# Performance work log

Measured on AMD Instinct MI355X. Metric: run time of the kernel, lower is better.

Reference implementation:

```python
import jax, jax.numpy as jnp
import numpy as np

P = 16  # num_partitions
DIN = 256  # in_features // P
DOUT = 256  # out_features // P

def setup_inputs() -> dict:
    key = jax.random.key(0)
    k1, k2, k3 = jax.random.split(key, 3)
    inputs = jax.random.normal(k1, (8, 2048, P * DIN), dtype=jnp.float32)
    weight = jax.random.normal(k2, (P, DOUT, DIN), dtype=jnp.float32) * (1.0 / np.sqrt(DIN))
    bias = jax.random.normal(k3, (P * DOUT,), dtype=jnp.float32) * (1.0 / np.sqrt(DIN))
    return {"inputs": inputs, "weight": weight, "bias": bias}

def reference(inputs, weight, bias):
    # inputs: (B, S, P*DIN) -> (B, S, P, DIN)
    x = inputs.reshape(*inputs.shape[:-1], P, DIN)
    # block-diagonal matmul: (B,S,P,DIN) x (P,DOUT,DIN) -> (B,S,P,DOUT)
    y = jnp.einsum('bspi,poi->bspo', x, weight)
    # transpose=True: swap (P, DOUT) -> (DOUT, P), then flatten
    y = jnp.swapaxes(y, -2, -1)
    y = y.reshape(*y.shape[:-2], DOUT * P)
    return y + bias
```

## Files before the change

kernel.cpp:

```cpp
#include <hip/hip_runtime.h>


typedef __attribute__((ext_vector_type(4))) float f32x4;
typedef __attribute__((ext_vector_type(8))) short short8;

#define LDS_ROW 8208
#define LDS_SIZE (16 * LDS_ROW)

__device__ __forceinline__ unsigned int pk2(float a, float b) {
  union { float f; unsigned int u; } x, y;
  x.f = a; y.f = b;
  unsigned int ua = x.u + (0x7fffu + ((x.u >> 16) & 1u));
  unsigned int ub = y.u + (0x7fffu + ((y.u >> 16) & 1u));
  return (ua >> 16) | (ub & 0xffff0000u);
}

__global__ __launch_bounds__(256) void wconv_kernel(
    const float* __restrict__ w, unsigned int* __restrict__ o) {
  int i = blockIdx.x * 256 + threadIdx.x;
  float4 f = ((const float4*)w)[i];
  uint2 u;
  u.x = pk2(f.x, f.y);
  u.y = pk2(f.z, f.w);
  ((uint2*)o)[i] = u;
}

__global__ __launch_bounds__(512, 2) void diag_gemm_kernel(
    const float* __restrict__ x, const unsigned short* __restrict__ wb,
    const float* __restrict__ bias, float* __restrict__ out) {
  extern __shared__ char lds[];
  const int tid = threadIdx.x;
  const int wv  = tid >> 6;
  const int l   = tid & 63;
  const long T0 = (long)blockIdx.x * 16;

  const int n  = l & 15;
  const int kg = l >> 4;

  const unsigned short* bbs0 = wb + (wv * 16 + n) * 256 + kg * 8;
  const unsigned short* bbs1 = wb + ((wv + 8) * 16 + n) * 256 + kg * 8;

  short8 a[2][8], b[2][8];

#pragma unroll
  for (int ks = 0; ks < 8; ++ks) b[0][ks] = *(const short8*)(bbs0 + ks * 32);

#pragma unroll
  for (int rr = 0; rr < 2; ++rr) {
    const int row = wv * 2 + rr;
    const float* src = x + (T0 + row) * 4096;
    char* dst = lds + row * LDS_ROW;
#pragma unroll
    for (int i = 0; i < 8; ++i) {
      int c = l + 64 * i;
      float4 f0 = ((const float4*)src)[2 * c];
      float4 f1 = ((const float4*)src)[2 * c + 1];
      uint4 u;
      u.x = pk2(f0.x, f0.y);
      u.y = pk2(f0.z, f0.w);
      u.z = pk2(f1.x, f1.y);
      u.w = pk2(f1.z, f1.w);
      *(uint4*)(dst + c * 16) = u;
    }
  }
  __syncthreads();

  const char* abase = lds + n * LDS_ROW + kg * 16;
#pragma unroll
  for (int ks = 0; ks < 8; ++ks) a[0][ks] = *(const short8*)(abase + ks * 64);

  float* obase = out + T0 * 4096;

#pragma unroll
  for (int s = 0; s < 2; ++s) {
    const int o0 = (wv + 8 * s) * 16;
    f32x4 res[16];

#pragma unroll
    for (int p = 0; p < 16; ++p) {
      const int g = s * 16 + p;
      const int cur = g & 1, nxt = cur ^ 1;
      if (g < 31) {
        const int gn = g + 1;
        const unsigned short* bp =
            ((gn & 16) ? bbs1 : bbs0) + (gn & 15) * 65536;
#pragma unroll
        for (int ks = 0; ks < 8; ++ks)
          b[nxt][ks] = *(const short8*)(bp + ks * 32);
        const char* ap = abase + (gn & 15) * 512;
#pragma unroll
        for (int ks = 0; ks < 8; ++ks)
          a[nxt][ks] = *(const short8*)(ap + ks * 64);
      }
      f32x4 acc = (f32x4){0.f, 0.f, 0.f, 0.f};
#pragma unroll
      for (int ks = 0; ks < 8; ++ks)
        acc = __builtin_amdgcn_mfma_f32_16x16x32_bf16(a[cur][ks], b[cur][ks],
                                                      acc, 0, 0, 0);
      res[p] = acc;
    }

    const float* bp2 = bias + (o0 + n) * 16;
    float4 bv0 = ((const float4*)bp2)[0];
    float4 bv1 = ((const float4*)bp2)[1];
    float4 bv2 = ((const float4*)bp2)[2];
    float4 bv3 = ((const float4*)bp2)[3];
    float* ob = obase + (long)(o0 + n) * 16;
#pragma unroll
    for (int r = 0; r < 4; ++r) {
      float* orow = ob + (long)(kg * 4 + r) * 4096;
      float4 v0 = make_float4(res[0][r] + bv0.x, res[1][r] + bv0.y,
                              res[2][r] + bv0.z, res[3][r] + bv0.w);
      float4 v1 = make_float4(res[4][r] + bv1.x, res[5][r] + bv1.y,
                              res[6][r] + bv1.z, res[7][r] + bv1.w);
      float4 v2 = make_float4(res[8][r] + bv2.x, res[9][r] + bv2.y,
                              res[10][r] + bv2.z, res[11][r] + bv2.w);
      float4 v3 = make_float4(res[12][r] + bv3.x, res[13][r] + bv3.y,
                              res[14][r] + bv3.z, res[15][r] + bv3.w);
      ((float4*)orow)[0] = v0;
      ((float4*)orow)[1] = v1;
      ((float4*)orow)[2] = v2;
      ((float4*)orow)[3] = v3;
    }
  }
}

extern "C" void kernel_launch(void* const* d_in, const int* in_sizes, int n_in,
                              void* d_out, int out_size, void* d_ws, size_t ws_size,
                              hipStream_t stream) {
  const float* x    = (const float*)d_in[0];
  const float* w    = (const float*)d_in[1];
  const float* bias = (const float*)d_in[2];
  float* out = (float*)d_out;
  unsigned int* wb = (unsigned int*)d_ws;

  (void)hipFuncSetAttribute((const void*)diag_gemm_kernel,
                            hipFuncAttributeMaxDynamicSharedMemorySize, LDS_SIZE);

  wconv_kernel<<<1024, 256, 0, stream>>>(w, wb);

  diag_gemm_kernel<<<1024, 512, LDS_SIZE, stream>>>(
      x, (const unsigned short*)wb, bias, out);
}
```

Baseline: 672.8 us.

## Stream fp32 activation slices into LDS via async DMA with a four-buffer ring

Instead of loading all 16 token rows to registers, converting them to bf16 and storing to LDS up front, the kernel now uses global_load_lds to DMA fp32 partition slices straight into a 4-deep LDS ring buffer. Each slice is prefetched three iterations ahead and synchronised with explicit vmcnt waits and barriers. Conversion to bf16 moves to the LDS-read side using the hardware v_cvt_pk_bf16_f32 instruction. Blocks shrink to 256 threads, with each wave covering 4 output groups. The aim is to overlap global activation loads with MFMA work and cut LDS footprint, at the cost of more barriers per block and more conversions per fragment read.

```diff
diff --git a/kernel.cpp b/kernel.cpp
--- a/kernel.cpp
+++ b/kernel.cpp
@@ -4,8 +4,10 @@
 typedef __attribute__((ext_vector_type(4))) float f32x4;
 typedef __attribute__((ext_vector_type(8))) short short8;
 
-#define LDS_ROW 8208
-#define LDS_SIZE (16 * LDS_ROW)
+#define SLICE_STRIDE 1040
+#define BUF_BYTES    (16 * SLICE_STRIDE)
+#define NBUF         4
+#define LDS_TOTAL    (NBUF * BUF_BYTES)
 
 __device__ __forceinline__ unsigned int pk2(float a, float b) {
   union { float f; unsigned int u; } x, y;
@@ -13,6 +15,18 @@
   unsigned int ua = x.u + (0x7fffu + ((x.u >> 16) & 1u));
   unsigned int ub = y.u + (0x7fffu + ((y.u >> 16) & 1u));
   return (ua >> 16) | (ub & 0xffff0000u);
+}
+
+__device__ __forceinline__ unsigned int cvtpk(float a, float b) {
+  unsigned int r;
+  asm("v_cvt_pk_bf16_f32 %0, %1, %2" : "=v"(r) : "v"(a), "v"(b));
+  return r;
+}
+
+__device__ __forceinline__ void dma_row(const float* g, char* l) {
+  __builtin_amdgcn_global_load_lds(
+      (const __attribute__((address_space(1))) unsigned int*)g,
+      (__attribute__((address_space(3))) unsigned int*)l, 16, 0, 0);
 }
 
 __global__ __launch_bounds__(256) void wconv_kernel(
@@ -25,7 +39,7 @@
   ((uint2*)o)[i] = u;
 }
 
-__global__ __launch_bounds__(512, 2) void diag_gemm_kernel(
+__global__ __launch_bounds__(256, 2) void diag_gemm_kernel(
     const float* __restrict__ x, const unsigned short* __restrict__ wb,
     const float* __restrict__ bias, float* __restrict__ out) {
   extern __shared__ char lds[];
@@ -37,69 +51,85 @@
   const int n  = l & 15;
   const int kg = l >> 4;
 
-  const unsigned short* bbs0 = wb + (wv * 16 + n) * 256 + kg * 8;
-  const unsigned short* bbs1 = wb + ((wv + 8) * 16 + n) * 256 + kg * 8;
+  const int C0 = (wv * 16 + n) * 256 + kg * 8;
+  const float* xrow0 = x + (T0 + wv * 4) * 4096 + l * 4;
 
-  short8 a[2][8], b[2][8];
+  short8 a[8], b[2][8];
 
 #pragma unroll
-  for (int ks = 0; ks < 8; ++ks) b[0][ks] = *(const short8*)(bbs0 + ks * 32);
-
+  for (int sl = 0; sl < 3; ++sl) {
 #pragma unroll
-  for (int rr = 0; rr < 2; ++rr) {
-    const int row = wv * 2 + rr;
-    const float* src = x + (T0 + row) * 4096;
-    char* dst = lds + row * LDS_ROW;
+    for (int i = 0; i < 4; ++i)
+      dma_row(xrow0 + i * 4096 + sl * 256,
+              lds + sl * BUF_BYTES + (wv * 4 + i) * SLICE_STRIDE);
+  }
+  __builtin_amdgcn_sched_barrier(0);
+  {
+    const unsigned short* bp = wb + C0;
 #pragma unroll
-    for (int i = 0; i < 8; ++i) {
-      int c = l + 64 * i;
-      float4 f0 = ((const float4*)src)[2 * c];
-      float4 f1 = ((const float4*)src)[2 * c + 1];
-      uint4 u;
-      u.x = pk2(f0.x, f0.y);
-      u.y = pk2(f0.z, f0.w);
-      u.z = pk2(f1.x, f1.y);
-      u.w = pk2(f1.z, f1.w);
-      *(uint4*)(dst + c * 16) = u;
-    }
+    for (int ks = 0; ks < 8; ++ks) b[0][ks] = *(const short8*)(bp + ks * 32);
   }
-  __syncthreads();
-
-  const char* abase = lds + n * LDS_ROW + kg * 16;
-#pragma unroll
-  for (int ks = 0; ks < 8; ++ks) a[0][ks] = *(const short8*)(abase + ks * 64);
+  __builtin_amdgcn_sched_barrier(0);
+  asm volatile("s_waitcnt vmcnt(16)" ::: "memory");
+  __builtin_amdgcn_s_barrier();
+  __builtin_amdgcn_sched_barrier(0);
 
   float* obase = out + T0 * 4096;
 
-#pragma unroll
-  for (int s = 0; s < 2; ++s) {
-    const int o0 = (wv + 8 * s) * 16;
+  for (int s = 0; s < 4; ++s) {
     f32x4 res[16];
-
 #pragma unroll
     for (int p = 0; p < 16; ++p) {
-      const int g = s * 16 + p;
-      const int cur = g & 1, nxt = cur ^ 1;
-      if (g < 31) {
-        const int gn = g + 1;
-        const unsigned short* bp =
-            ((gn & 16) ? bbs1 : bbs0) + (gn & 15) * 65536;
+      const int cur = p & 1, nxt = cur ^ 1;
+
+      const char* ab = lds + (p & 3) * BUF_BYTES + n * SLICE_STRIDE + kg * 32;
 #pragma unroll
-        for (int ks = 0; ks < 8; ++ks)
-          b[nxt][ks] = *(const short8*)(bp + ks * 32);
-        const char* ap = abase + (gn & 15) * 512;
+      for (int ks = 0; ks < 8; ++ks) {
+        f32x4 lo = *(const f32x4*)(ab + ks * 128);
+        f32x4 hi = *(const f32x4*)(ab + ks * 128 + 16);
+        union { unsigned int u[4]; short8 s8; } t;
+        t.u[0] = cvtpk(lo[0], lo[1]);
+        t.u[1] = cvtpk(lo[2], lo[3]);
+        t.u[2] = cvtpk(hi[0], hi[1]);
+        t.u[3] = cvtpk(hi[2], hi[3]);
+        a[ks] = t.s8;
+      }
+
+      if (p != 15) {
+        const unsigned short* bp = wb + C0 + s * 16384 + (p + 1) * 65536;
 #pragma unroll
-        for (int ks = 0; ks < 8; ++ks)
-          a[nxt][ks] = *(const short8*)(ap + ks * 64);
+        for (int ks = 0; ks < 8; ++ks) b[nxt][ks] = *(const short8*)(bp + ks * 32);
+      } else if (s != 3) {
+        const unsigned short* bp = wb + C0 + (s + 1) * 16384;
+#pragma unroll
+        for (int ks = 0; ks < 8; ++ks) b[nxt][ks] = *(const short8*)(bp + ks * 32);
       }
-      f32x4 acc = (f32x4){0.f, 0.f, 0.f, 0.f};
+
+      if (p < 13 || s != 3) {
+        const int p3 = (p + 3) & 15;
+#pragma unroll
+        for (int i = 0; i < 4; ++i)
+          dma_row(xrow0 + i * 4096 + p3 * 256,
+                  lds + ((p + 3) & 3) * BUF_BYTES + (wv * 4 + i) * SLICE_STRIDE);
+      }
+
+      f32x4 acc = {0.f, 0.f, 0.f, 0.f};
 #pragma unroll
       for (int ks = 0; ks < 8; ++ks)
-        acc = __builtin_amdgcn_mfma_f32_16x16x32_bf16(a[cur][ks], b[cur][ks],
-                                                      acc, 0, 0, 0);
+        acc = __builtin_amdgcn_mfma_f32_16x16x32_bf16(a[ks], b[cur][ks], acc, 0, 0, 0);
       res[p] = acc;
+
+      if (!(p == 15 && s == 3)) {
+        __builtin_amdgcn_sched_barrier(0);
+        if (p == 13 && s == 3)      asm volatile("s_waitcnt vmcnt(12)" ::: "memory");
+        else if (p == 14 && s == 3) asm volatile("s_waitcnt vmcnt(8)"  ::: "memory");
+        else                        asm volatile("s_waitcnt vmcnt(16)" ::: "memory");
+        __builtin_amdgcn_s_barrier();
+        __builtin_amdgcn_sched_barrier(0);
+      }
     }
 
+    const int o0 = (wv + 4 * s) * 16;
     const float* bp2 = bias + (o0 + n) * 16;
     float4 bv0 = ((const float4*)bp2)[0];
     float4 bv1 = ((const float4*)bp2)[1];
@@ -135,10 +165,10 @@
   unsigned int* wb = (unsigned int*)d_ws;
 
   (void)hipFuncSetAttribute((const void*)diag_gemm_kernel,
-                            hipFuncAttributeMaxDynamicSharedMemorySize, LDS_SIZE);
+                            hipFuncAttributeMaxDynamicSharedMemorySize, LDS_TOTAL);
 
   wconv_kernel<<<1024, 256, 0, stream>>>(w, wb);
 
-  diag_gemm_kernel<<<1024, 512, LDS_SIZE, stream>>>(
+  diag_gemm_kernel<<<1024, 256, LDS_TOTAL, stream>>>(
       x, (const unsigned short*)wb, bias, out);
 }
```

Result: slower. 719.1 us (+6.9%).
